# Kernel tuning notes

Measured on AMD Instinct MI355X. Metric: run time of the kernel, lower is better.

## Reference

```python
import jax, jax.numpy as jnp
import numpy as np

N = 20000; E = 320000; G = 64; IN = 64; HID = 128; H = 8; HD = H * HID  # 1024


def setup_inputs() -> dict:
    key = jax.random.key(0)
    ks = jax.random.split(key, 32)
    inp = {}
    inp['x'] = jax.random.normal(ks[0], (N, IN), jnp.float32)
    inp['edge_index'] = jax.random.randint(ks[1], (2, E), 0, N, dtype=jnp.int64)
    inp['batch'] = jnp.sort(jax.random.randint(ks[2], (N,), 0, G, dtype=jnp.int64))
    dims_in = [IN, HD, HD]
    k = 3
    for i in range(3):
        d_in = dims_in[i]
        inp[f'gat_W{i}'] = jax.random.normal(ks[k], (d_in, HD), jnp.float32) * (1.0 / np.sqrt(d_in)); k += 1
        inp[f'gat_b{i}'] = jnp.zeros((HD,), jnp.float32)
        inp[f'att_src{i}'] = jax.random.normal(ks[k], (H, HID), jnp.float32) * 0.1; k += 1
        inp[f'att_dst{i}'] = jax.random.normal(ks[k], (H, HID), jnp.float32) * 0.1; k += 1
    for i in range(2):
        inp[f'boot_W{i}'] = jax.random.normal(ks[k], (HD, HD), jnp.float32) * (1.0 / np.sqrt(HD)); k += 1
        inp[f'boot_b{i}'] = jnp.zeros((HD,), jnp.float32)
    inp['clf_W1'] = jax.random.normal(ks[k], (HD, HID), jnp.float32) * (1.0 / np.sqrt(HD)); k += 1
    inp['clf_b1'] = jnp.zeros((HID,), jnp.float32)
    inp['clf_W2'] = jax.random.normal(ks[k], (HID, 2), jnp.float32) * (1.0 / np.sqrt(HID)); k += 1
    inp['clf_b2'] = jnp.zeros((2,), jnp.float32)
    return inp


def _gat_layer(x, W, b, a_src, a_dst, src, dst):
    # PyG GATConv (concat=True, self-loops already appended, eval mode => no dropout)
    h = (x @ W).reshape(N, H, HID)                      # [N,H,D]
    s = jnp.einsum('nhd,hd->nh', h, a_src)              # [N,H]
    t = jnp.einsum('nhd,hd->nh', h, a_dst)              # [N,H]
    e = jax.nn.leaky_relu(s[src] + t[dst], 0.2)         # [Etot,H]
    m = jax.ops.segment_max(e, dst, num_segments=N)     # segment softmax over incoming edges
    m = jnp.where(jnp.isfinite(m), m, 0.0)
    ex = jnp.exp(e - m[dst])
    denom = jax.ops.segment_sum(ex, dst, num_segments=N)
    alpha = ex / jnp.maximum(denom[dst], 1e-16)         # [Etot,H]
    out = jax.ops.segment_sum(alpha[:, :, None] * h[src], dst, num_segments=N)  # [N,H,D]
    return out.reshape(N, HD) + b


def reference(x, edge_index, batch,
              gat_W0, gat_b0, att_src0, att_dst0,
              gat_W1, gat_b1, att_src1, att_dst1,
              gat_W2, gat_b2, att_src2, att_dst2,
              boot_W0, boot_b0, boot_W1, boot_b1,
              clf_W1, clf_b1, clf_W2, clf_b2):
    loop = jnp.arange(N, dtype=edge_index.dtype)
    src = jnp.concatenate([edge_index[0], loop])
    dst = jnp.concatenate([edge_index[1], loop])
    gat = [(gat_W0, gat_b0, att_src0, att_dst0),
           (gat_W1, gat_b1, att_src1, att_dst1),
           (gat_W2, gat_b2, att_src2, att_dst2)]
    boot = [(boot_W0, boot_b0), (boot_W1, boot_b1)]
    h = x
    for i in range(3):
        W, b, a_s, a_d = gat[i]
        h = jax.nn.elu(_gat_layer(h, W, b, a_s, a_d, src, dst))
        if i < 2:
            noise = jax.random.normal(jax.random.key(100 + i), h.shape, h.dtype) * 0.1
            bW, bb = boot[i]
            h = (h + noise) @ bW + bb
    # global mean pool over graphs
    sums = jax.ops.segment_sum(h, batch, num_segments=G)        # [G,HD]
    cnts = jax.ops.segment_sum(jnp.ones((N,), h.dtype), batch, num_segments=G)
    g = sums / jnp.maximum(cnts, 1.0)[:, None]
    z = jax.nn.relu(g @ clf_W1 + clf_b1)                        # dropout = identity (eval)
    return z @ clf_W2 + clf_b2
```

## Files before the change

kernel.cpp:

```cpp
#include <hip/hip_runtime.h>
#include <stdint.h>

#define N_NODES 20000
#define N_EDGES 320000
#define E_TOT   (N_EDGES + N_NODES)
#define NGRAPH  64
#define DIN     64
#define DHID    128
#define NHEAD   8
#define HDIM    1024

typedef unsigned int u32;
typedef unsigned short u16;
typedef __bf16 bfx8 __attribute__((ext_vector_type(8)));
typedef float f32x4 __attribute__((ext_vector_type(4)));
typedef float f32x2 __attribute__((ext_vector_type(2)));

__device__ __forceinline__ u16 f2bf(float f){
  u32 u = __float_as_uint(f);
  u32 r = (u + 0x7FFFu + ((u >> 16) & 1u)) >> 16;
  return (u16)r;
}
__device__ __forceinline__ float bf2f(u16 v){
  return __uint_as_float(((u32)v) << 16);
}
__device__ __forceinline__ f32x2 up2(u32 u){
  f32x2 v;
  v.x = __uint_as_float(u << 16);
  v.y = __uint_as_float(u & 0xffff0000u);
  return v;
}

typedef __attribute__((address_space(3))) u32 lds_u32_t;
typedef const __attribute__((address_space(1))) u32 glb_u32_t;
__device__ __forceinline__ void g2l16(const void* g, void* l){
  __builtin_amdgcn_global_load_lds((glb_u32_t*)(uintptr_t)g,
                                   (lds_u32_t*)(uintptr_t)l, 16, 0, 0);
}

__device__ __forceinline__ u32 rotl32(u32 x, int r){ return (x<<r) | (x>>(32-r)); }

__device__ __forceinline__ void threefry2x32(u32 k0, u32 k1, u32 x0, u32 x1,
                                             u32& y0, u32& y1){
  u32 k2 = k0 ^ k1 ^ 0x1BD11BDAu;
  x0 += k0; x1 += k1;
#define TFR(r) { x0 += x1; x1 = rotl32(x1, (r)); x1 ^= x0; }
  TFR(13) TFR(15) TFR(26) TFR(6)
  x0 += k1; x1 += k2 + 1u;
  TFR(17) TFR(29) TFR(16) TFR(24)
  x0 += k2; x1 += k0 + 2u;
  TFR(13) TFR(15) TFR(26) TFR(6)
  x0 += k0; x1 += k1 + 3u;
  TFR(17) TFR(29) TFR(16) TFR(24)
  x0 += k1; x1 += k2 + 4u;
  TFR(13) TFR(15) TFR(26) TFR(6)
  x0 += k2; x1 += k0 + 5u;
#undef TFR
  y0 = x0; y1 = x1;
}

__device__ __forceinline__ float erfinv_fast(float x){
  float t = fmaf(-x, x, 1.0f);
  float w = -__logf(t);
  float p;
  if (w < 5.0f){
    w -= 2.5f;
    p = 2.81022636e-08f;
    p = fmaf(p, w, 3.43273939e-07f);
    p = fmaf(p, w, -3.5233877e-06f);
    p = fmaf(p, w, -4.39150654e-06f);
    p = fmaf(p, w, 0.00021858087f);
    p = fmaf(p, w, -0.00125372503f);
    p = fmaf(p, w, -0.00417768164f);
    p = fmaf(p, w, 0.246640727f);
    p = fmaf(p, w, 1.50140941f);
  } else {
    w = sqrtf(w) - 3.0f;
    p = -0.000200214257f;
    p = fmaf(p, w, 0.000100950558f);
    p = fmaf(p, w, 0.00134934322f);
    p = fmaf(p, w, -0.00367342844f);
    p = fmaf(p, w, 0.00573950773f);
    p = fmaf(p, w, -0.0076224613f);
    p = fmaf(p, w, 0.00943887047f);
    p = fmaf(p, w, 1.00167406f);
    p = fmaf(p, w, 2.83297682f);
  }
  return p * x;
}

__device__ __forceinline__ float jax_normal(u32 seed, u32 i){
  u32 y0, y1;
  threefry2x32(0u, seed, 0u, i, y0, y1);
  u32 bits = y0 ^ y1;
  float f = __uint_as_float((bits >> 9) | 0x3f800000u) - 1.0f;
  float xx = fmaxf(-0.99999994f, fmaf(f, 2.0f, -0.99999994f));
  return 1.41421356f * erfinv_fast(xx);
}

__global__ __launch_bounds__(256) void prep_misc_kernel(const float* __restrict__ x,
    const float* __restrict__ W0, const float* __restrict__ W1,
    u16* __restrict__ xbf, u16* __restrict__ O0, u16* __restrict__ O1,
    const int* __restrict__ ei, const int* __restrict__ batch,
    int* __restrict__ cnt, int* __restrict__ gcnt){
  const int z = blockIdx.y;
  if (z < 3){
    const float* S = (z==0) ? W0 : (z==1) ? W1 : x;
    u16* D = (z==0) ? O0 : (z==1) ? O1 : xbf;
    const int total = (z==2) ? N_NODES*DIN : HDIM*HDIM;
    int i = (blockIdx.x*256 + threadIdx.x)*4;
    if (i < total){
      float4 v = *(const float4*)(S + i);
      D[i+0] = f2bf(v.x); D[i+1] = f2bf(v.y);
      D[i+2] = f2bf(v.z); D[i+3] = f2bf(v.w);
    }
  } else {
    int i = blockIdx.x*256 + threadIdx.x;
    if (i < N_EDGES) atomicAdd(&cnt[ei[N_EDGES + i]], 1);
    else if (i < E_TOT) atomicAdd(&gcnt[batch[i - N_EDGES]], 1);
  }
}

__global__ __launch_bounds__(256) void transpose_all_kernel(
    const float* __restrict__ W0, const float* __restrict__ W1,
    const float* __restrict__ W2,
    u16* __restrict__ T0, u16* __restrict__ T1, u16* __restrict__ T2){
  const int z = blockIdx.z;
  const float* W = (z==0)?W0:(z==1)?W1:W2;
  u16* T = (z==0)?T0:(z==1)?T1:T2;
  const int K = (z==0)?DIN:HDIM;
  const int bk = blockIdx.y*32;
  if (bk >= K) return;
  __shared__ float t[32][33];
  int bn = blockIdx.x*32;
  int lx = threadIdx.x & 31, ly = threadIdx.x >> 5;
#pragma unroll
  for (int r = 0; r < 32; r += 8)
    t[ly+r][lx] = W[(size_t)(bk+ly+r)*HDIM + bn + lx];
  __syncthreads();
#pragma unroll
  for (int r = 0; r < 32; r += 8)
    T[(size_t)(bn+ly+r)*K + bk + lx] = f2bf(t[lx][ly+r]);
}

__global__ __launch_bounds__(1024) void scan_pair_kernel(const int* __restrict__ cnt,
    int* __restrict__ rowptr, int* __restrict__ cursor, int* __restrict__ colidx,
    const int* __restrict__ gcnt, int* __restrict__ goff){
  if (blockIdx.x == 1){
    if (threadIdx.x == 0){
      int s = 0;
      for (int g = 0; g < NGRAPH; ++g){ goff[g] = s; s += gcnt[g]; }
      goff[NGRAPH] = s;
    }
    return;
  }
  __shared__ int wsum[16];
  __shared__ int carry_s;
  const int tid = threadIdx.x, lane = tid & 63, wv = tid >> 6;
  if (tid == 0){ carry_s = 0; rowptr[0] = 0; }
  __syncthreads();
  for (int base = 0; base < N_NODES; base += 1024){
    int i = base + tid;
    int v = (i < N_NODES) ? cnt[i] + 1 : 0;
    int s = v;
#pragma unroll
    for (int off = 1; off < 64; off <<= 1){
      int t = __shfl_up(s, off);
      if (lane >= off) s += t;
    }
    if (lane == 63) wsum[wv] = s;
    __syncthreads();
    if (wv == 0 && lane < 16){
      int ws = wsum[lane];
#pragma unroll
      for (int off = 1; off < 16; off <<= 1){
        int t = __shfl_up(ws, off);
        if (lane >= off) ws += t;
      }
      wsum[lane] = ws;
    }
    __syncthreads();
    int incl = s + ((wv > 0) ? wsum[wv-1] : 0) + carry_s;
    if (i < N_NODES){
      rowptr[i+1] = incl;
      const int slot = incl - v;
      colidx[slot] = i;
      cursor[i] = slot + 1;
    }
    __syncthreads();
    if (tid == 1023) carry_s = incl;
    __syncthreads();
  }
}

__global__ __launch_bounds__(256) void fill_edges_kernel(const int* __restrict__ ei,
    int* __restrict__ cursor, int* __restrict__ colidx){
  int e = blockIdx.x*256 + threadIdx.x;
  if (e < N_EDGES){
    int s = ei[e], d = ei[N_EDGES + e];
    int p = atomicAdd(&cursor[d], 1);
    colidx[p] = s;
  }
}

__device__ __forceinline__ void gemm_tile(const u16* __restrict__ A,
    const u16* __restrict__ BT, const float* __restrict__ bias,
    u16* __restrict__ Cb, int M, int K, int bm, int bn,
    u16* As, u16* Bs,
    const float* __restrict__ asrc, const float* __restrict__ adst,
    float* __restrict__ sbuf, float* __restrict__ tbuf){
  const int tid = threadIdx.x;
  const int lane = tid & 63, w = tid >> 6;
  const int wm = (w & 1)*64, wn = (w >> 1)*64;

  const int cid0 = tid, cid1 = 256 + tid;
  const int r0 = cid0 & 127, kc0 = cid0 >> 7;
  const int r1 = cid1 & 127, kc1 = cid1 >> 7;
  int ar0 = bm + r0; if (ar0 >= M) ar0 = M - 1;
  int ar1 = bm + r1; if (ar1 >= M) ar1 = M - 1;
  const u16* ag0 = A + (size_t)ar0*K + kc0*8;
  const u16* ag1 = A + (size_t)ar1*K + kc1*8;
  const u16* bg0 = BT + (size_t)(bn + r0)*K + kc0*8;
  const u16* bg1 = BT + (size_t)(bn + r1)*K + kc1*8;
  u16* al0 = As + cid0*8;  u16* al1 = As + cid1*8;
  u16* bl0 = Bs + cid0*8;  u16* bl1 = Bs + cid1*8;

  const int rowl = lane & 15, kg = lane >> 4;
  const bfx8* ap = (const bfx8*)(As + ((size_t)kg*128 + wm + rowl)*8);
  const bfx8* bp = (const bfx8*)(Bs + ((size_t)kg*128 + wn + rowl)*8);

  f32x4 acc[4][4] = {};
  for (int k0 = 0; k0 < K; k0 += 32){
    g2l16(ag0 + k0, al0);
    g2l16(ag1 + k0, al1);
    g2l16(bg0 + k0, bl0);
    g2l16(bg1 + k0, bl1);
    __syncthreads();
    bfx8 af[4], bfr[4];
#pragma unroll
    for (int i = 0; i < 4; ++i){ af[i] = ap[i*16]; bfr[i] = bp[i*16]; }
#pragma unroll
    for (int i = 0; i < 4; ++i)
#pragma unroll
      for (int j = 0; j < 4; ++j)
        acc[j][i] = __builtin_amdgcn_mfma_f32_16x16x32_bf16(bfr[j], af[i], acc[j][i], 0, 0, 0);
    __syncthreads();
  }

  const int quad = lane >> 4;
  const bool dost = (sbuf != nullptr);
  const int head = bn >> 7;
  float sl[4] = {0.f,0.f,0.f,0.f}, tl[4] = {0.f,0.f,0.f,0.f};
#pragma unroll
  for (int j = 0; j < 4; ++j){
    const int col0 = bn + wn + j*16 + quad*4;
    float4 bv = make_float4(0.f,0.f,0.f,0.f);
    if (bias) bv = *(const float4*)(bias + col0);
    float4 av = make_float4(0.f,0.f,0.f,0.f), dv = av;
    if (dost){
      const int d0 = col0 - bn;
      av = *(const float4*)(asrc + head*DHID + d0);
      dv = *(const float4*)(adst + head*DHID + d0);
    }
#pragma unroll
    for (int i = 0; i < 4; ++i){
      const int row = bm + wm + i*16 + rowl;
      const u16 p0 = f2bf(acc[j][i][0] + bv.x);
      const u16 p1 = f2bf(acc[j][i][1] + bv.y);
      const u16 p2 = f2bf(acc[j][i][2] + bv.z);
      const u16 p3 = f2bf(acc[j][i][3] + bv.w);
      if (row < M){
        uint2 pk;
        pk.x = (u32)p0 | ((u32)p1 << 16);
        pk.y = (u32)p2 | ((u32)p3 << 16);
        *(uint2*)(Cb + (size_t)row*HDIM + col0) = pk;
      }
      if (dost){
        const float c0 = bf2f(p0), c1 = bf2f(p1), c2 = bf2f(p2), c3 = bf2f(p3);
        sl[i] = fmaf(c0, av.x, fmaf(c1, av.y, fmaf(c2, av.z, fmaf(c3, av.w, sl[i]))));
        tl[i] = fmaf(c0, dv.x, fmaf(c1, dv.y, fmaf(c2, dv.z, fmaf(c3, dv.w, tl[i]))));
      }
    }
  }
  if (dost){
#pragma unroll
    for (int i = 0; i < 4; ++i){
      sl[i] += __shfl_xor(sl[i], 16); sl[i] += __shfl_xor(sl[i], 32);
      tl[i] += __shfl_xor(tl[i], 16); tl[i] += __shfl_xor(tl[i], 32);
    }
    float* sred = (float*)As;
    float* tred = sred + 128;
    if ((w >> 1) == 0 && quad == 0){
#pragma unroll
      for (int i = 0; i < 4; ++i){
        const int rl = wm + i*16 + rowl;
        sred[rl] = sl[i]; tred[rl] = tl[i];
      }
    }
    __syncthreads();
    if ((w >> 1) == 1 && quad == 0){
#pragma unroll
      for (int i = 0; i < 4; ++i){
        const int rl = wm + i*16 + rowl;
        const int row = bm + rl;
        if (row < M){
          sbuf[row*NHEAD + head] = sred[rl] + sl[i];
          tbuf[row*NHEAD + head] = tred[rl] + tl[i];
        }
      }
    }
  }
}

__global__ __launch_bounds__(256) void gemm_bf16(
    const u16* __restrict__ A, const u16* __restrict__ BT,
    const float* __restrict__ bias, u16* __restrict__ Cb, int M, int K,
    const float* __restrict__ asrc, const float* __restrict__ adst,
    float* __restrict__ sbuf, float* __restrict__ tbuf){
  __shared__ __align__(16) u16 As[4*128*8];
  __shared__ __align__(16) u16 Bs[4*128*8];
  const int kblk = blockIdx.y*8 + blockIdx.x;
  const int xc = kblk & 7, bq = (kblk >> 3) & 7, gq = kblk >> 6;
  const int bmi = gq*8 + xc;
  const int mt = (M + 127) >> 7;
  if (bmi >= mt) return;
  gemm_tile(A, BT, bias, Cb, M, K, bmi*128, bq*128, As, Bs,
            asrc, adst, sbuf, tbuf);
}

__global__ __launch_bounds__(256) void wf_bias_kernel(
    const u16* __restrict__ A0, const u16* __restrict__ B0, u16* __restrict__ C0,
    const u16* __restrict__ A1, const u16* __restrict__ B1, u16* __restrict__ C1,
    const float* __restrict__ bb0, const u16* __restrict__ gwt0,
    const float* __restrict__ bb1, const u16* __restrict__ gwt1,
    float* __restrict__ fb0, float* __restrict__ fb1){
  __shared__ __align__(16) u16 As[4*128*8];
  __shared__ __align__(16) u16 Bs[4*128*8];
  if (blockIdx.z < 2){
    const u16* A = blockIdx.z ? A1 : A0;
    const u16* B = blockIdx.z ? B1 : B0;
    u16* C = blockIdx.z ? C1 : C0;
    gemm_tile(A, B, nullptr, C, HDIM, HDIM, blockIdx.y*128, blockIdx.x*128,
              As, Bs, nullptr, nullptr, nullptr, nullptr);
  } else {
    const int kb = blockIdx.y*8 + blockIdx.x;
    const int wv = threadIdx.x >> 6, lane = threadIdx.x & 63;
    for (int idx = kb*4 + wv; idx < 2*HDIM; idx += 256){
      const int set = idx >> 10, n = idx & (HDIM-1);
      const float* bb = set ? bb1 : bb0;
      const u16* row = (set ? gwt1 : gwt0) + (size_t)n*HDIM + lane*16;
      const float* bp = bb + lane*16;
      float acc = 0.f;
#pragma unroll
      for (int k = 0; k < 16; ++k) acc = fmaf(bp[k], bf2f(row[k]), acc);
      for (int off = 32; off > 0; off >>= 1) acc += __shfl_down(acc, off);
      if (lane == 0) (set ? fb1 : fb0)[n] = acc;
    }
  }
}

__global__ __launch_bounds__(256) void gat_agg_kernel(const u16* __restrict__ hlin,
    const float* __restrict__ sbuf, const float* __restrict__ tbuf,
    const int* __restrict__ rowptr, const int* __restrict__ colidx,
    const float* __restrict__ bias, float* __restrict__ outf,
    u16* __restrict__ outbf, u32 seed){
  const int tid  = threadIdx.x;
  const int lane = tid & 63;
  const int n    = blockIdx.x*4 + (tid >> 6);
  const int jsub = lane >> 3;
  const int hh   = lane & 7;
  const int hA   = lane >> 3;
  const int row0 = rowptr[n];
  const int deg  = rowptr[n+1] - row0;
  const float tn = tbuf[n*NHEAD + hh];
  const char* hl = (const char*)hlin;
  const u32 lb   = (u32)lane << 5;

  f32x2 acc[8] = {};
  float m_run = -INFINITY, d_run = 0.f;

  for (int c = 0; c < deg; c += 8){
    const int ne = min(8, deg - c);
    const int jj = (jsub < ne) ? jsub : (ne - 1);
    const int srcv = colidx[row0 + c + jj];
    float e = sbuf[srcv*NHEAD + hh] + tn;
    e = (e > 0.f) ? e : 0.2f*e;
    if (jsub >= ne) e = -INFINITY;
    float mc = e;
    mc = fmaxf(mc, __shfl_xor(mc, 8));
    mc = fmaxf(mc, __shfl_xor(mc, 16));
    mc = fmaxf(mc, __shfl_xor(mc, 32));
    const float mnew = fmaxf(m_run, mc);
    const float w = __expf(e - mnew);
    float ws = w;
    ws += __shfl_xor(ws, 8);
    ws += __shfl_xor(ws, 16);
    ws += __shfl_xor(ws, 32);
    const float r = (m_run == -INFINITY) ? 0.0f : __expf(m_run - mnew);
    d_run = fmaf(d_run, r, ws);
    m_run = mnew;
    const float rA = __shfl(r, hA);
    const f32x2 r2 = {rA, rA};
#pragma unroll
    for (int q = 0; q < 8; ++q) acc[q] *= r2;
    int j = 0;
    for (; j + 2 <= ne; j += 2){
      const int s0 = __builtin_amdgcn_readlane(srcv, j*8);
      const int s1 = __builtin_amdgcn_readlane(srcv, j*8 + 8);
      const float w0 = __shfl(w, j*8 + hA);
      const float w1 = __shfl(w, j*8 + 8 + hA);
      const char* rp0 = hl + (((size_t)(u32)s0) << 11);
      const char* rp1 = hl + (((size_t)(u32)s1) << 11);
      const uint4 a0 = *(const uint4*)(rp0 + lb);
      const uint4 a1 = *(const uint4*)(rp0 + lb + 16);
      const uint4 b0 = *(const uint4*)(rp1 + lb);
      const uint4 b1 = *(const uint4*)(rp1 + lb + 16);
      const f32x2 w02 = {w0, w0}, w12 = {w1, w1};
      acc[0] = __builtin_elementwise_fma(w02, up2(a0.x), acc[0]);
      acc[1] = __builtin_elementwise_fma(w02, up2(a0.y), acc[1]);
      acc[2] = __builtin_elementwise_fma(w02, up2(a0.z), acc[2]);
      acc[3] = __builtin_elementwise_fma(w02, up2(a0.w), acc[3]);
      acc[4] = __builtin_elementwise_fma(w02, up2(a1.x), acc[4]);
      acc[5] = __builtin_elementwise_fma(w02, up2(a1.y), acc[5]);
      acc[6] = __builtin_elementwise_fma(w02, up2(a1.z), acc[6]);
      acc[7] = __builtin_elementwise_fma(w02, up2(a1.w), acc[7]);
      acc[0] = __builtin_elementwise_fma(w12, up2(b0.x), acc[0]);
      acc[1] = __builtin_elementwise_fma(w12, up2(b0.y), acc[1]);
      acc[2] = __builtin_elementwise_fma(w12, up2(b0.z), acc[2]);
      acc[3] = __builtin_elementwise_fma(w12, up2(b0.w), acc[3]);
      acc[4] = __builtin_elementwise_fma(w12, up2(b1.x), acc[4]);
      acc[5] = __builtin_elementwise_fma(w12, up2(b1.y), acc[5]);
      acc[6] = __builtin_elementwise_fma(w12, up2(b1.z), acc[6]);
      acc[7] = __builtin_elementwise_fma(w12, up2(b1.w), acc[7]);
    }
    if (j < ne){
      const int s0 = __builtin_amdgcn_readlane(srcv, j*8);
      const float w0 = __shfl(w, j*8 + hA);
      const char* rp0 = hl + (((size_t)(u32)s0) << 11);
      const uint4 a0 = *(const uint4*)(rp0 + lb);
      const uint4 a1 = *(const uint4*)(rp0 + lb + 16);
      const f32x2 w02 = {w0, w0};
      acc[0] = __builtin_elementwise_fma(w02, up2(a0.x), acc[0]);
      acc[1] = __builtin_elementwise_fma(w02, up2(a0.y), acc[1]);
      acc[2] = __builtin_elementwise_fma(w02, up2(a0.z), acc[2]);
      acc[3] = __builtin_elementwise_fma(w02, up2(a0.w), acc[3]);
      acc[4] = __builtin_elementwise_fma(w02, up2(a1.x), acc[4]);
      acc[5] = __builtin_elementwise_fma(w02, up2(a1.y), acc[5]);
      acc[6] = __builtin_elementwise_fma(w02, up2(a1.z), acc[6]);
      acc[7] = __builtin_elementwise_fma(w02, up2(a1.w), acc[7]);
    }
  }

  const float dA = __shfl(d_run, hA);
  const float invA = 1.0f / fmaxf(dA, 1e-16f);
  float o[16];
#pragma unroll
  for (int q = 0; q < 8; ++q){ o[2*q] = acc[q].x; o[2*q+1] = acc[q].y; }
  const float4* bp = (const float4*)(bias + lane*16);
#pragma unroll
  for (int q = 0; q < 4; ++q){
    const float4 bv = bp[q];
    o[4*q+0] = fmaf(o[4*q+0], invA, bv.x);
    o[4*q+1] = fmaf(o[4*q+1], invA, bv.y);
    o[4*q+2] = fmaf(o[4*q+2], invA, bv.z);
    o[4*q+3] = fmaf(o[4*q+3], invA, bv.w);
  }
#pragma unroll
  for (int k = 0; k < 16; ++k)
    o[k] = (o[k] > 0.f) ? o[k] : __expf(o[k]) - 1.0f;
  if (outbf){
    const u32 ib = (u32)n*HDIM + (u32)lane*16u;
    u32 pk[8];
#pragma unroll
    for (int q = 0; q < 8; ++q){
      const float v0 = fmaf(0.1f, jax_normal(seed, ib + 2u*q + 0u), o[2*q+0]);
      const float v1 = fmaf(0.1f, jax_normal(seed, ib + 2u*q + 1u), o[2*q+1]);
      pk[q] = (u32)f2bf(v0) | ((u32)f2bf(v1) << 16);
    }
    uint4* dst = (uint4*)(outbf + (size_t)n*HDIM + lane*16);
    dst[0] = make_uint4(pk[0], pk[1], pk[2], pk[3]);
    dst[1] = make_uint4(pk[4], pk[5], pk[6], pk[7]);
  } else {
    float4* dst = (float4*)(outf + (size_t)n*HDIM + lane*16);
#pragma unroll
    for (int q = 0; q < 4; ++q)
      dst[q] = make_float4(o[4*q], o[4*q+1], o[4*q+2], o[4*q+3]);
  }
}

__global__ __launch_bounds__(256) void pool_sum_kernel(const float* __restrict__ h,
    const int* __restrict__ batch, float* __restrict__ gsum){
  const int n0 = blockIdx.x*128;
  const int n1 = min(n0 + 128, N_NODES);
  const int cb = threadIdx.x*4;
  float4 acc = make_float4(0.f,0.f,0.f,0.f);
  int curg = batch[n0];
  for (int n = n0; n < n1; ++n){
    const int g = batch[n];
    if (g != curg){
      atomicAdd(&gsum[curg*HDIM + cb+0], acc.x);
      atomicAdd(&gsum[curg*HDIM + cb+1], acc.y);
      atomicAdd(&gsum[curg*HDIM + cb+2], acc.z);
      atomicAdd(&gsum[curg*HDIM + cb+3], acc.w);
      acc = make_float4(0.f,0.f,0.f,0.f);
      curg = g;
    }
    const float4 v = *(const float4*)(h + (size_t)n*HDIM + cb);
    acc.x += v.x; acc.y += v.y; acc.z += v.z; acc.w += v.w;
  }
  atomicAdd(&gsum[curg*HDIM + cb+0], acc.x);
  atomicAdd(&gsum[curg*HDIM + cb+1], acc.y);
  atomicAdd(&gsum[curg*HDIM + cb+2], acc.z);
  atomicAdd(&gsum[curg*HDIM + cb+3], acc.w);
}

__global__ __launch_bounds__(256) void pool_clf_kernel(const float* __restrict__ gsum,
    const int* __restrict__ gcnt,
    const float* __restrict__ W1, const float* __restrict__ b1,
    const float* __restrict__ W2, const float* __restrict__ b2,
    float* __restrict__ out){
  __shared__ float gs[HDIM];
  __shared__ float z[DHID];
  const int g = blockIdx.x, tid = threadIdx.x;
  const int cb = tid*4;
  const float invc = 1.0f / fmaxf((float)gcnt[g], 1.0f);
  const float4 s = *(const float4*)(gsum + (size_t)g*HDIM + cb);
  gs[cb+0] = s.x*invc; gs[cb+1] = s.y*invc;
  gs[cb+2] = s.z*invc; gs[cb+3] = s.w*invc;
  __syncthreads();
  if (tid < DHID){
    float a = b1[tid];
    for (int k = 0; k < HDIM; ++k) a = fmaf(gs[k], W1[k*DHID + tid], a);
    z[tid] = fmaxf(a, 0.0f);
  }
  __syncthreads();
  if (tid < 2){
    float o = b2[tid];
    for (int k = 0; k < DHID; ++k) o = fmaf(z[k], W2[k*2 + tid], o);
    out[g*2 + tid] = o;
  }
}

extern "C" void kernel_launch(void* const* d_in, const int* in_sizes, int n_in,
                              void* d_out, int out_size, void* d_ws, size_t ws_size,
                              hipStream_t stream){
  const float* x      = (const float*)d_in[0];
  const int*   ei     = (const int*)d_in[1];
  const int*   batch  = (const int*)d_in[2];
  const float* gatW[3]  = {(const float*)d_in[3],  (const float*)d_in[7],  (const float*)d_in[11]};
  const float* gatB[3]  = {(const float*)d_in[4],  (const float*)d_in[8],  (const float*)d_in[12]};
  const float* asrc[3]  = {(const float*)d_in[5],  (const float*)d_in[9],  (const float*)d_in[13]};
  const float* adst[3]  = {(const float*)d_in[6],  (const float*)d_in[10], (const float*)d_in[14]};
  const float* bootW[2] = {(const float*)d_in[15], (const float*)d_in[17]};
  const float* bootB[2] = {(const float*)d_in[16], (const float*)d_in[18]};
  const float* clfW1 = (const float*)d_in[19];
  const float* clfb1 = (const float*)d_in[20];
  const float* clfW2 = (const float*)d_in[21];
  const float* clfb2 = (const float*)d_in[22];
  float* outp = (float*)d_out;

  float* fws  = (float*)d_ws;
  float* hB   = fws;
  float* sbuf = hB + (size_t)N_NODES*HDIM;
  float* tbuf = sbuf + (size_t)N_NODES*NHEAD;
  float* fbias0 = tbuf + (size_t)N_NODES*NHEAD;
  float* fbias1 = fbias0 + HDIM;
  u16* xbf    = (u16*)(fbias1 + HDIM);
  u16* hAbf   = xbf + (size_t)N_NODES*DIN;
  u16* hBbf   = hAbf + (size_t)N_NODES*HDIM;
  u16* wt[3];
  wt[0] = hBbf + (size_t)N_NODES*HDIM;
  wt[1] = wt[0] + (size_t)HDIM*DIN;
  wt[2] = wt[1] + (size_t)HDIM*HDIM;
  u16* wnt0   = wt[2] + (size_t)HDIM*HDIM;
  u16* wnt1   = wnt0 + (size_t)HDIM*HDIM;
  u16* wf0    = wnt1 + (size_t)HDIM*HDIM;
  u16* wf1    = wf0 + (size_t)HDIM*HDIM;
  int* rowptr = (int*)(wf1 + (size_t)HDIM*HDIM);
  int* cursor = rowptr + (N_NODES+1);
  int* colidx = cursor + N_NODES;
  int* gcnt   = colidx + E_TOT;
  int* cnt    = gcnt + NGRAPH;
  float* gsum = (float*)(cnt + N_NODES);
  int* goff   = (int*)(gsum + (size_t)NGRAPH*HDIM);

  (void)hipMemsetAsync(gcnt, 0, (NGRAPH + N_NODES + NGRAPH*HDIM)*sizeof(int), stream);

  const int nb_e = (N_EDGES + 255)/256;

  prep_misc_kernel<<<dim3((E_TOT + 255)/256, 4), 256, 0, stream>>>(
      x, bootW[0], bootW[1], xbf, wnt0, wnt1, ei, batch, cnt, gcnt);
  transpose_all_kernel<<<dim3(HDIM/32, HDIM/32, 3), 256, 0, stream>>>(
      gatW[0], gatW[1], gatW[2], wt[0], wt[1], wt[2]);
  scan_pair_kernel<<<2, 1024, 0, stream>>>(cnt, rowptr, cursor, colidx, gcnt, goff);
  fill_edges_kernel<<<nb_e, 256, 0, stream>>>(ei, cursor, colidx);

  wf_bias_kernel<<<dim3(8, 8, 3), 256, 0, stream>>>(
      wt[1], wnt0, wf0, wt[2], wnt1, wf1,
      bootB[0], wt[1], bootB[1], wt[2], fbias0, fbias1);

  const int mt = (N_NODES + 127)/128;
  dim3 gemmGrid(8, (mt + 7)/8*8);

  gemm_bf16<<<gemmGrid, 256, 0, stream>>>(xbf, wt[0], nullptr, hAbf, N_NODES, DIN,
                                          asrc[0], adst[0], sbuf, tbuf);
  gat_agg_kernel<<<N_NODES/4, 256, 0, stream>>>(hAbf, sbuf, tbuf, rowptr, colidx,
                                                gatB[0], nullptr, hBbf, 100u);
  gemm_bf16<<<gemmGrid, 256, 0, stream>>>(hBbf, wf0, fbias0, hAbf, N_NODES, HDIM,
                                          asrc[1], adst[1], sbuf, tbuf);
  gat_agg_kernel<<<N_NODES/4, 256, 0, stream>>>(hAbf, sbuf, tbuf, rowptr, colidx,
                                                gatB[1], nullptr, hBbf, 101u);
  gemm_bf16<<<gemmGrid, 256, 0, stream>>>(hBbf, wf1, fbias1, hAbf, N_NODES, HDIM,
                                          asrc[2], adst[2], sbuf, tbuf);
  gat_agg_kernel<<<N_NODES/4, 256, 0, stream>>>(hAbf, sbuf, tbuf, rowptr, colidx,
                                                gatB[2], hB, nullptr, 0u);

  pool_sum_kernel<<<(N_NODES + 127)/128, 256, 0, stream>>>(hB, batch, gsum);
  pool_clf_kernel<<<NGRAPH, 256, 0, stream>>>(gsum, gcnt,
                                              clfW1, clfb1, clfW2, clfb2, outp);
}
```

Measured before the change: 873.0 us.

## Reorder first GAT layer to aggregate raw features before projection

For layer 0, the attention logits are computed straight from x using precomputed W0·a_src/a_dst vectors. Neighbours' 64-dim input features are then aggregated per head, and the per-head aggregate is multiplied by W0 afterwards. The split-bf16 hi/lo trick keeps precision, and a duplicated weight with K=128 makes this work. This replaces gathering 1024-dim projected rows per edge with gathering 64-dim rows, cutting edge-gather traffic, and it fuses ELU and noise into the GEMM epilogue. The cost is an extra per-head GEMM stage and a different rounding order.

```diff
diff --git a/kernel.cpp b/kernel.cpp
--- a/kernel.cpp
+++ b/kernel.cpp
@@ -102,7 +102,9 @@
     const float* __restrict__ W0, const float* __restrict__ W1,
     u16* __restrict__ xbf, u16* __restrict__ O0, u16* __restrict__ O1,
     const int* __restrict__ ei, const int* __restrict__ batch,
-    int* __restrict__ cnt, int* __restrict__ gcnt){
+    int* __restrict__ cnt, int* __restrict__ gcnt,
+    const float* __restrict__ gatW0, const float* __restrict__ asrc0,
+    const float* __restrict__ adst0, float* __restrict__ wst){
   const int z = blockIdx.y;
   if (z < 3){
     const float* S = (z==0) ? W0 : (z==1) ? W1 : x;
@@ -114,10 +116,49 @@
       D[i+0] = f2bf(v.x); D[i+1] = f2bf(v.y);
       D[i+2] = f2bf(v.z); D[i+3] = f2bf(v.w);
     }
-  } else {
+  } else if (z == 3){
     int i = blockIdx.x*256 + threadIdx.x;
     if (i < N_EDGES) atomicAdd(&cnt[ei[N_EDGES + i]], 1);
     else if (i < E_TOT) atomicAdd(&gcnt[batch[i - N_EDGES]], 1);
+  } else {
+    if (blockIdx.x == 0){
+      for (int o = threadIdx.x; o < DIN*16; o += 256){
+        const int d = o >> 4, c = o & 15;
+        const int hh = c & 7;
+        const float* av = ((c < 8) ? asrc0 : adst0) + hh*DHID;
+        const float* wr = gatW0 + (size_t)d*HDIM + hh*DHID;
+        float a = 0.f;
+        for (int k = 0; k < DHID; ++k) a = fmaf(wr[k], av[k], a);
+        wst[o] = a;
+      }
+    }
+  }
+}
+
+__global__ __launch_bounds__(256) void st0_kernel(const float* __restrict__ x,
+    const float* __restrict__ wst, float* __restrict__ sbuf,
+    float* __restrict__ tbuf){
+  const int n = blockIdx.x*256 + threadIdx.x;
+  if (n >= N_NODES) return;
+  float acc[16];
+#pragma unroll
+  for (int c = 0; c < 16; ++c) acc[c] = 0.f;
+  const float* xr = x + (size_t)n*DIN;
+  for (int d = 0; d < DIN; d += 4){
+    const float4 xv = *(const float4*)(xr + d);
+    const float* w0 = wst + d*16;
+#pragma unroll
+    for (int c = 0; c < 16; ++c){
+      acc[c] = fmaf(xv.x, w0[c],      acc[c]);
+      acc[c] = fmaf(xv.y, w0[16+c],   acc[c]);
+      acc[c] = fmaf(xv.z, w0[32+c],   acc[c]);
+      acc[c] = fmaf(xv.w, w0[48+c],   acc[c]);
+    }
+  }
+#pragma unroll
+  for (int h = 0; h < NHEAD; ++h){
+    sbuf[n*NHEAD + h] = acc[h];
+    tbuf[n*NHEAD + h] = acc[8 + h];
   }
 }
 
@@ -139,8 +180,15 @@
     t[ly+r][lx] = W[(size_t)(bk+ly+r)*HDIM + bn + lx];
   __syncthreads();
 #pragma unroll
-  for (int r = 0; r < 32; r += 8)
-    T[(size_t)(bn+ly+r)*K + bk + lx] = f2bf(t[lx][ly+r]);
+  for (int r = 0; r < 32; r += 8){
+    const u16 v = f2bf(t[lx][ly+r]);
+    if (z == 0){
+      const size_t base = (size_t)(bn+ly+r)*128 + bk + lx;
+      T[base] = v; T[base + 64] = v;
+    } else {
+      T[(size_t)(bn+ly+r)*K + bk + lx] = v;
+    }
+  }
 }
 
 __global__ __launch_bounds__(1024) void scan_pair_kernel(const int* __restrict__ cnt,
@@ -208,7 +256,8 @@
     u16* __restrict__ Cb, int M, int K, int bm, int bn,
     u16* As, u16* Bs,
     const float* __restrict__ asrc, const float* __restrict__ adst,
-    float* __restrict__ sbuf, float* __restrict__ tbuf){
+    float* __restrict__ sbuf, float* __restrict__ tbuf,
+    const int emode, const u32 seed){
   const int tid = threadIdx.x;
   const int lane = tid & 63, w = tid >> 6;
   const int wm = (w & 1)*64, wn = (w >> 1)*64;
@@ -265,20 +314,42 @@
 #pragma unroll
     for (int i = 0; i < 4; ++i){
       const int row = bm + wm + i*16 + rowl;
-      const u16 p0 = f2bf(acc[j][i][0] + bv.x);
-      const u16 p1 = f2bf(acc[j][i][1] + bv.y);
-      const u16 p2 = f2bf(acc[j][i][2] + bv.z);
-      const u16 p3 = f2bf(acc[j][i][3] + bv.w);
-      if (row < M){
-        uint2 pk;
-        pk.x = (u32)p0 | ((u32)p1 << 16);
-        pk.y = (u32)p2 | ((u32)p3 << 16);
-        *(uint2*)(Cb + (size_t)row*HDIM + col0) = pk;
-      }
-      if (dost){
-        const float c0 = bf2f(p0), c1 = bf2f(p1), c2 = bf2f(p2), c3 = bf2f(p3);
-        sl[i] = fmaf(c0, av.x, fmaf(c1, av.y, fmaf(c2, av.z, fmaf(c3, av.w, sl[i]))));
-        tl[i] = fmaf(c0, dv.x, fmaf(c1, dv.y, fmaf(c2, dv.z, fmaf(c3, dv.w, tl[i]))));
+      if (emode == 1){
+        if (row < M){
+          float v0 = acc[j][i][0] + bv.x;
+          float v1 = acc[j][i][1] + bv.y;
+          float v2 = acc[j][i][2] + bv.z;
+          float v3 = acc[j][i][3] + bv.w;
+          v0 = (v0 > 0.f) ? v0 : __expf(v0) - 1.0f;
+          v1 = (v1 > 0.f) ? v1 : __expf(v1) - 1.0f;
+          v2 = (v2 > 0.f) ? v2 : __expf(v2) - 1.0f;
+          v3 = (v3 > 0.f) ? v3 : __expf(v3) - 1.0f;
+          const u32 ib = (u32)row*HDIM + (u32)col0;
+          v0 = fmaf(0.1f, jax_normal(seed, ib+0u), v0);
+          v1 = fmaf(0.1f, jax_normal(seed, ib+1u), v1);
+          v2 = fmaf(0.1f, jax_normal(seed, ib+2u), v2);
+          v3 = fmaf(0.1f, jax_normal(seed, ib+3u), v3);
+          uint2 pk;
+          pk.x = (u32)f2bf(v0) | ((u32)f2bf(v1) << 16);
+          pk.y = (u32)f2bf(v2) | ((u32)f2bf(v3) << 16);
+          *(uint2*)(Cb + (size_t)row*HDIM + col0) = pk;
+        }
+      } else {
+        const u16 p0 = f2bf(acc[j][i][0] + bv.x);
+        const u16 p1 = f2bf(acc[j][i][1] + bv.y);
+        const u16 p2 = f2bf(acc[j][i][2] + bv.z);
+        const u16 p3 = f2bf(acc[j][i][3] + bv.w);
+        if (row < M){
+          uint2 pk;
+          pk.x = (u32)p0 | ((u32)p1 << 16);
+          pk.y = (u32)p2 | ((u32)p3 << 16);
+          *(uint2*)(Cb + (size_t)row*HDIM + col0) = pk;
+        }
+        if (dost){
+          const float c0 = bf2f(p0), c1 = bf2f(p1), c2 = bf2f(p2), c3 = bf2f(p3);
+          sl[i] = fmaf(c0, av.x, fmaf(c1, av.y, fmaf(c2, av.z, fmaf(c3, av.w, sl[i]))));
+          tl[i] = fmaf(c0, dv.x, fmaf(c1, dv.y, fmaf(c2, dv.z, fmaf(c3, dv.w, tl[i]))));
+        }
       }
     }
   }
@@ -325,7 +396,19 @@
   const int mt = (M + 127) >> 7;
   if (bmi >= mt) return;
   gemm_tile(A, BT, bias, Cb, M, K, bmi*128, bq*128, As, Bs,
-            asrc, adst, sbuf, tbuf);
+            asrc, adst, sbuf, tbuf, 0, 0u);
+}
+
+__global__ __launch_bounds__(256) void gemm_l0t(
+    const u16* __restrict__ agg2, const u16* __restrict__ BT,
+    const float* __restrict__ bias, u16* __restrict__ Cb, u32 seed){
+  __shared__ __align__(16) u16 As[4*128*8];
+  __shared__ __align__(16) u16 Bs[4*128*8];
+  const int head = blockIdx.x;
+  const int bm = blockIdx.y*128;
+  gemm_tile(agg2 + (size_t)head*N_NODES*128, BT, bias, Cb, N_NODES, 128,
+            bm, head*128, As, Bs, nullptr, nullptr, nullptr, nullptr,
+            1, seed);
 }
 
 __global__ __launch_bounds__(256) void wf_bias_kernel(
@@ -341,7 +424,7 @@
     const u16* B = blockIdx.z ? B1 : B0;
     u16* C = blockIdx.z ? C1 : C0;
     gemm_tile(A, B, nullptr, C, HDIM, HDIM, blockIdx.y*128, blockIdx.x*128,
-              As, Bs, nullptr, nullptr, nullptr, nullptr);
+              As, Bs, nullptr, nullptr, nullptr, nullptr, 0, 0u);
   } else {
     const int kb = blockIdx.y*8 + blockIdx.x;
     const int wv = threadIdx.x >> 6, lane = threadIdx.x & 63;
@@ -488,6 +571,98 @@
   }
 }
 
+__global__ __launch_bounds__(256) void agg_x_kernel(const u16* __restrict__ xbf,
+    const float* __restrict__ sbuf, const float* __restrict__ tbuf,
+    const int* __restrict__ rowptr, const int* __restrict__ colidx,
+    u16* __restrict__ agg2){
+  const int tid  = threadIdx.x;
+  const int lane = tid & 63;
+  const int n    = blockIdx.x*4 + (tid >> 6);
+  const int jsub = lane >> 3;
+  const int hh   = lane & 7;
+  const int hA   = lane >> 3;
+  const int row0 = rowptr[n];
+  const int deg  = rowptr[n+1] - row0;
+  const float tn = tbuf[n*NHEAD + hh];
+  const char* xb = (const char*)xbf;
+  const u32 lb   = (u32)(lane & 7) << 4;
+
+  f32x2 acc[4] = {};
+  float m_run = -INFINITY, d_run = 0.f;
+
+  for (int c = 0; c < deg; c += 8){
+    const int ne = min(8, deg - c);
+    const int jj = (jsub < ne) ? jsub : (ne - 1);
+    const int srcv = colidx[row0 + c + jj];
+    float e = sbuf[srcv*NHEAD + hh] + tn;
+    e = (e > 0.f) ? e : 0.2f*e;
+    if (jsub >= ne) e = -INFINITY;
+    float mc = e;
+    mc = fmaxf(mc, __shfl_xor(mc, 8));
+    mc = fmaxf(mc, __shfl_xor(mc, 16));
+    mc = fmaxf(mc, __shfl_xor(mc, 32));
+    const float mnew = fmaxf(m_run, mc);
+    const float w = __expf(e - mnew);
+    float ws = w;
+    ws += __shfl_xor(ws, 8);
+    ws += __shfl_xor(ws, 16);
+    ws += __shfl_xor(ws, 32);
+    const float r = (m_run == -INFINITY) ? 0.0f : __expf(m_run - mnew);
+    d_run = fmaf(d_run, r, ws);
+    m_run = mnew;
+    const float rA = __shfl(r, hA);
+    const f32x2 r2 = {rA, rA};
+#pragma unroll
+    for (int q = 0; q < 4; ++q) acc[q] *= r2;
+    int j = 0;
+    for (; j + 2 <= ne; j += 2){
+      const int s0 = __builtin_amdgcn_readlane(srcv, j*8);
+      const int s1 = __builtin_amdgcn_readlane(srcv, j*8 + 8);
+      const float w0 = __shfl(w, j*8 + hA);
+      const float w1 = __shfl(w, j*8 + 8 + hA);
+      const uint4 a0 = *(const uint4*)(xb + (((size_t)(u32)s0) << 7) + lb);
+      const uint4 b0 = *(const uint4*)(xb + (((size_t)(u32)s1) << 7) + lb);
+      const f32x2 w02 = {w0, w0}, w12 = {w1, w1};
+      acc[0] = __builtin_elementwise_fma(w02, up2(a0.x), acc[0]);
+      acc[1] = __builtin_elementwise_fma(w02, up2(a0.y), acc[1]);
+      acc[2] = __builtin_elementwise_fma(w02, up2(a0.z), acc[2]);
+      acc[3] = __builtin_elementwise_fma(w02, up2(a0.w), acc[3]);
+      acc[0] = __builtin_elementwise_fma(w12, up2(b0.x), acc[0]);
+      acc[1] = __builtin_elementwise_fma(w12, up2(b0.y), acc[1]);
+      acc[2] = __builtin_elementwise_fma(w12, up2(b0.z), acc[2]);
+      acc[3] = __builtin_elementwise_fma(w12, up2(b0.w), acc[3]);
+    }
+    if (j < ne){
+      const int s0 = __builtin_amdgcn_readlane(srcv, j*8);
+      const float w0 = __shfl(w, j*8 + hA);
+      const uint4 a0 = *(const uint4*)(xb + (((size_t)(u32)s0) << 7) + lb);
+      const f32x2 w02 = {w0, w0};
+      acc[0] = __builtin_elementwise_fma(w02, up2(a0.x), acc[0]);
+      acc[1] = __builtin_elementwise_fma(w02, up2(a0.y), acc[1]);
+      acc[2] = __builtin_elementwise_fma(w02, up2(a0.z), acc[2]);
+      acc[3] = __builtin_elementwise_fma(w02, up2(a0.w), acc[3]);
+    }
+  }
+
+  const float dA = __shfl(d_run, hA);
+  const float invA = 1.0f / fmaxf(dA, 1e-16f);
+  float v[8];
+#pragma unroll
+  for (int q = 0; q < 4; ++q){ v[2*q] = acc[q].x*invA; v[2*q+1] = acc[q].y*invA; }
+  u32 hp[4], lp[4];
+#pragma unroll
+  for (int q = 0; q < 4; ++q){
+    const u16 h0 = f2bf(v[2*q]),   h1 = f2bf(v[2*q+1]);
+    const u16 l0 = f2bf(v[2*q]   - bf2f(h0));
+    const u16 l1 = f2bf(v[2*q+1] - bf2f(h1));
+    hp[q] = (u32)h0 | ((u32)h1 << 16);
+    lp[q] = (u32)l0 | ((u32)l1 << 16);
+  }
+  u16* base = agg2 + ((size_t)hA*N_NODES + (size_t)n)*128 + (lane & 7)*8;
+  *(uint4*)(base)      = make_uint4(hp[0], hp[1], hp[2], hp[3]);
+  *(uint4*)(base + 64) = make_uint4(lp[0], lp[1], lp[2], lp[3]);
+}
+
 __global__ __launch_bounds__(256) void pool_sum_kernel(const float* __restrict__ h,
     const int* __restrict__ batch, float* __restrict__ gsum){
   const int n0 = blockIdx.x*128;
@@ -570,7 +745,7 @@
   u16* hBbf   = hAbf + (size_t)N_NODES*HDIM;
   u16* wt[3];
   wt[0] = hBbf + (size_t)N_NODES*HDIM;
-  wt[1] = wt[0] + (size_t)HDIM*DIN;
+  wt[1] = wt[0] + (size_t)HDIM*128;
   wt[2] = wt[1] + (size_t)HDIM*HDIM;
   u16* wnt0   = wt[2] + (size_t)HDIM*HDIM;
   u16* wnt1   = wnt0 + (size_t)HDIM*HDIM;
@@ -583,13 +758,18 @@
   int* cnt    = gcnt + NGRAPH;
   float* gsum = (float*)(cnt + N_NODES);
   int* goff   = (int*)(gsum + (size_t)NGRAPH*HDIM);
+  float* wst  = (float*)(goff + NGRAPH + 1);
+
+  u16* agg2 = hAbf;
 
   (void)hipMemsetAsync(gcnt, 0, (NGRAPH + N_NODES + NGRAPH*HDIM)*sizeof(int), stream);
 
   const int nb_e = (N_EDGES + 255)/256;
 
-  prep_misc_kernel<<<dim3((E_TOT + 255)/256, 4), 256, 0, stream>>>(
-      x, bootW[0], bootW[1], xbf, wnt0, wnt1, ei, batch, cnt, gcnt);
+  prep_misc_kernel<<<dim3((E_TOT + 255)/256, 5), 256, 0, stream>>>(
+      x, bootW[0], bootW[1], xbf, wnt0, wnt1, ei, batch, cnt, gcnt,
+      gatW[0], asrc[0], adst[0], wst);
+  st0_kernel<<<(N_NODES + 255)/256, 256, 0, stream>>>(x, wst, sbuf, tbuf);
   transpose_all_kernel<<<dim3(HDIM/32, HDIM/32, 3), 256, 0, stream>>>(
       gatW[0], gatW[1], gatW[2], wt[0], wt[1], wt[2]);
   scan_pair_kernel<<<2, 1024, 0, stream>>>(cnt, rowptr, cursor, colidx, gcnt, goff);
@@ -602,10 +782,10 @@
   const int mt = (N_NODES + 127)/128;
   dim3 gemmGrid(8, (mt + 7)/8*8);
 
-  gemm_bf16<<<gemmGrid, 256, 0, stream>>>(xbf, wt[0], nullptr, hAbf, N_NODES, DIN,
-                                          asrc[0], adst[0], sbuf, tbuf);
-  gat_agg_kernel<<<N_NODES/4, 256, 0, stream>>>(hAbf, sbuf, tbuf, rowptr, colidx,
-                                                gatB[0], nullptr, hBbf, 100u);
+  agg_x_kernel<<<N_NODES/4, 256, 0, stream>>>(xbf, sbuf, tbuf, rowptr, colidx,
+                                              agg2);
+  gemm_l0t<<<dim3(8, mt), 256, 0, stream>>>(agg2, wt[0], gatB[0], hBbf, 100u);
+
   gemm_bf16<<<gemmGrid, 256, 0, stream>>>(hBbf, wf0, fbias0, hAbf, N_NODES, HDIM,
                                           asrc[1], adst[1], sbuf, tbuf);
   gat_agg_kernel<<<N_NODES/4, 256, 0, stream>>>(hAbf, sbuf, tbuf, rowptr, colidx,
```

New measurement: 870.0 us. About the same (-0.4%).
